# Performance work log

Measured on AMD Instinct MI355X. Metric: run time of the kernel, lower is better.

Reference implementation:

```python
import jax, jax.numpy as jnp
import numpy as np
from jax import lax

EPS = 2.220446049250313e-16  # np.finfo(float).eps, used in SparseDispatcher.combine
TOP_K = 2
LOSS_COEF = 1e-2


def _conv7(x, w, groups):
    # x: [B,C,H,W], w: [O, C//groups, 7, 7], 'same' padding
    return lax.conv_general_dilated(
        x, w, window_strides=(1, 1), padding=[(3, 3), (3, 3)],
        dimension_numbers=("NCHW", "OIHW", "NCHW"), feature_group_count=groups)


def setup_inputs() -> dict:
    key = jax.random.key(0)
    ks = jax.random.split(key, 8)
    B, C, H, E = 16, 64, 128, 8
    x = jax.random.normal(ks[0], (B, C, H, H), dtype=jnp.float32)
    # router: Conv2d(dim, 1, 7, padding=3)
    router_w = jax.random.normal(ks[1], (1, C, 7, 7), dtype=jnp.float32) * 0.05
    router_b = jnp.zeros((1,), dtype=jnp.float32)
    # gating weight: [weight_h*weight_h, num_experts] (small random so top-k is meaningful)
    w_gate = jax.random.normal(ks[2], (H * H, E), dtype=jnp.float32) * 0.01
    # experts: depthwise Conv2d(dim, dim, 7, groups=dim) per expert
    expert_w = jax.random.normal(ks[3], (E, C, 1, 7, 7), dtype=jnp.float32) * 0.05
    expert_b = jnp.zeros((E, C), dtype=jnp.float32)
    # shared expert: same depthwise conv
    shared_w = jax.random.normal(ks[4], (C, 1, 7, 7), dtype=jnp.float32) * 0.05
    shared_b = jnp.zeros((C,), dtype=jnp.float32)
    return dict(x=x, router_w=router_w, router_b=router_b, w_gate=w_gate,
                expert_w=expert_w, expert_b=expert_b,
                shared_w=shared_w, shared_b=shared_b)


def reference(x, router_w, router_b, w_gate, expert_w, expert_b, shared_w, shared_b):
    B, C, H, W = x.shape
    E = w_gate.shape[1]

    # ---- router + top-k gating (noisy_gating=False path) ----
    r = _conv7(x, router_w, groups=1) + router_b[None, :, None, None]   # [B,1,H,W]
    r_flat = r.reshape(B, H * W)                                        # [B,HW]
    logits = r_flat @ w_gate                                            # [B,E]
    top_logits, top_idx = lax.top_k(logits, min(TOP_K + 1, E))
    top_k_gates = jax.nn.softmax(top_logits[:, :TOP_K], axis=1)         # [B,k]
    gates = jnp.zeros((B, E), logits.dtype).at[
        jnp.arange(B)[:, None], top_idx[:, :TOP_K]].set(top_k_gates)     # [B,E]

    importance = gates.sum(0)
    load = (gates > 0).sum(0).astype(jnp.float32)

    def cv_sq(v):  # torch .var() is unbiased -> ddof=1
        return jnp.var(v, ddof=1) / (jnp.mean(v) ** 2 + 1e-10)

    loss = (cv_sq(importance) + cv_sq(load)) * LOSS_COEF

    # ---- experts: depthwise 7x7 conv per expert ----
    out = jax.vmap(lambda w, b: _conv7(x, w, C) + b[None, :, None, None])(
        expert_w, expert_b)                                             # [E,B,C,H,W]
    out = out.reshape(E, B, C, H * W).transpose(0, 1, 3, 2)             # [E,B,HW,C]

    # ---- SparseDispatcher.combine (multiply_by_gates=False): log-sum-exp over
    # selected experts only. Dense masked form == gather/scatter form exactly. ----
    mask = (gates > 0).T[:, :, None, None].astype(out.dtype)            # [E,B,1,1]
    combined = jnp.sum(jnp.exp(out) * mask, axis=0)                     # [B,HW,C]
    combined = jnp.where(combined == 0, EPS, combined)
    y = jnp.log(combined)

    # ---- shared expert ----
    shared = (_conv7(x, shared_w, C) + shared_b[None, :, None, None])
    shared = shared.reshape(B, C, H * W).transpose(0, 2, 1)             # [B,HW,C]

    return y + shared, loss
```

## Files before the change

### kernel.cpp

```cpp
#include <hip/hip_runtime.h>
#include <hip/hip_bf16.h>

#define B_  16
#define C_  64
#define H_  128
#define W_  128
#define HW_ (H_*W_)
#define E_  8

#define WS_LOGITS 0
#define WS_SEL    128
#define WS_PART   256

__global__ void k_sentinel(float* out, float v){
    if (blockIdx.x == 0 && threadIdx.x == 0) out[0] = v;
}

#define R_TH 16
#define R_TW 64
#define R_HH (R_TH+6)
#define R_HW (R_TW+6)
#define R_LS 76
#define R_HN (R_HH*R_HW)
#define RG_CH 8
#define RG_N  8

__device__ __forceinline__ void r_stage(const float* __restrict__ xc, float* dst,
                                        int row0, int col0, int tid){
    for (int i = tid; i < R_HN; i += 256){
        int hr = i / R_HW, hc = i - hr*R_HW;
        int gr = row0 + hr - 3, gc = col0 + hc - 3;
        float v = 0.f;
        if ((unsigned)gr < (unsigned)H_ && (unsigned)gc < (unsigned)W_)
            v = xc[gr*W_+gc];
        dst[hr*R_LS+hc] = v;
    }
}

__global__ __launch_bounds__(256) void k1p(const float* __restrict__ x,
                                           const float* __restrict__ rw,
                                           const float* __restrict__ rb,
                                           const float* __restrict__ wg,
                                           float* __restrict__ partial){
    __shared__ __align__(16) float tile[2][R_HH*R_LS];
    __shared__ float pred[4][E_];

    int id = blockIdx.x;
    int g   = id & 7; id >>= 3;
    int txt = id & 1; id >>= 1;
    int tyt = id & 7; id >>= 3;
    int b   = id;
    int row0 = tyt*R_TH, col0 = txt*R_TW;
    int tx = threadIdx.x & 15, ty = threadIdx.x >> 4;
    int row  = row0 + ty;
    int colb = col0 + 4*tx;

    const float* xg  = x  + ((size_t)(b*C_) + g*RG_CH)*HW_;
    const float* wgr = rw + g*RG_CH*49;

    float acc[4] = {0.f,0.f,0.f,0.f};

    r_stage(xg, tile[0], row0, col0, threadIdx.x);
    __syncthreads();

    for (int ch = 0; ch < RG_CH; ++ch){
        if (ch + 1 < RG_CH)
            r_stage(xg + (size_t)(ch+1)*HW_, tile[(ch+1)&1], row0, col0, threadIdx.x);

        const float* wr = wgr + ch*49;
        const float* tb = tile[ch&1];
        #pragma unroll
        for (int ky = 0; ky < 7; ++ky){
            const float* trp = &tb[(ty+ky)*R_LS + 4*tx];
            float4 va = *(const float4*)(trp);
            float4 vb = *(const float4*)(trp+4);
            float2 vc = *(const float2*)(trp+8);
            float win[10] = {va.x,va.y,va.z,va.w, vb.x,vb.y,vb.z,vb.w, vc.x,vc.y};
            #pragma unroll
            for (int kx = 0; kx < 7; ++kx){
                float w = wr[ky*7+kx];
                acc[0] += w*win[kx+0];
                acc[1] += w*win[kx+1];
                acc[2] += w*win[kx+2];
                acc[3] += w*win[kx+3];
            }
        }
        __syncthreads();
    }

    if (g == 0){
        float rbv = rb[0];
        acc[0]+=rbv; acc[1]+=rbv; acc[2]+=rbv; acc[3]+=rbv;
    }

    const float* wrow = wg + (size_t)(row*W_ + colb)*E_;
    float pl[E_];
    #pragma unroll
    for (int e = 0; e < E_; ++e) pl[e] = 0.f;
    #pragma unroll
    for (int p = 0; p < 4; ++p){
        float4 wa = *(const float4*)(wrow + p*E_);
        float4 wb = *(const float4*)(wrow + p*E_ + 4);
        float a = acc[p];
        pl[0] += a*wa.x; pl[1] += a*wa.y; pl[2] += a*wa.z; pl[3] += a*wa.w;
        pl[4] += a*wb.x; pl[5] += a*wb.y; pl[6] += a*wb.z; pl[7] += a*wb.w;
    }
    #pragma unroll
    for (int off = 32; off > 0; off >>= 1){
        #pragma unroll
        for (int e = 0; e < E_; ++e) pl[e] += __shfl_down(pl[e], off, 64);
    }
    int lane = threadIdx.x & 63, wv = threadIdx.x >> 6;
    if (lane == 0){
        #pragma unroll
        for (int e = 0; e < E_; ++e) pred[wv][e] = pl[e];
    }
    __syncthreads();
    if (threadIdx.x < E_){
        int e = threadIdx.x;
        float s = pred[0][e] + pred[1][e] + pred[2][e] + pred[3][e];
        partial[(size_t)blockIdx.x*E_ + e] = s;
    }
}

__global__ void k2_gating(const float* __restrict__ partial,
                          int* __restrict__ sel,
                          float* __restrict__ out){
    __shared__ float lg[B_*E_];
    __shared__ float g1s[B_], g2s[B_];
    __shared__ int   i1s[B_], i2s[B_];
    __shared__ float impS[E_], cntS[E_];
    int t = threadIdx.x;
    if (t < B_*E_){
        int b = t >> 3, e = t & 7;
        const float* pp = partial + ((size_t)b*128)*E_ + e;
        float s = 0.f;
        #pragma unroll 4
        for (int j = 0; j < 128; ++j) s += pp[(size_t)j*E_];
        lg[t] = s;
    }
    __syncthreads();
    if (t < B_){
        const float* l = lg + t*E_;
        int i1 = 0;
        #pragma unroll
        for (int e = 1; e < E_; ++e) if (l[e] > l[i1]) i1 = e;
        int i2 = (i1 == 0) ? 1 : 0;
        #pragma unroll
        for (int e = 0; e < E_; ++e) if (e != i1 && l[e] > l[i2]) i2 = e;
        float ex = expf(l[i2] - l[i1]);
        float g1 = 1.f/(1.f+ex), g2 = ex/(1.f+ex);
        sel[t] = i1; sel[B_ + t] = i2;
        g1s[t] = g1; g2s[t] = g2; i1s[t] = i1; i2s[t] = i2;
    }
    __syncthreads();
    if (t < E_){
        float im = 0.f, cn = 0.f;
        #pragma unroll
        for (int bb = 0; bb < B_; ++bb){
            im += (i1s[bb]==t ? g1s[bb] : 0.f) + (i2s[bb]==t ? g2s[bb] : 0.f);
            cn += (i1s[bb]==t ? 1.f : 0.f)     + (i2s[bb]==t ? 1.f : 0.f);
        }
        impS[t] = im; cntS[t] = cn;
    }
    __syncthreads();
    if (t == 0){
        float m1 = 0.f, m2 = 0.f;
        for (int e = 0; e < E_; ++e){ m1 += impS[e]; m2 += cntS[e]; }
        m1 *= (1.f/E_); m2 *= (1.f/E_);
        float v1 = 0.f, v2 = 0.f;
        for (int e = 0; e < E_; ++e){
            float d1 = impS[e] - m1; v1 += d1*d1;
            float d2 = cntS[e] - m2; v2 += d2*d2;
        }
        v1 *= (1.f/(E_-1)); v2 *= (1.f/(E_-1));
        float loss = (v1/(m1*m1 + 1e-10f) + v2/(m2*m2 + 1e-10f)) * 0.01f;
        out[(size_t)B_*HW_*C_] = loss;
    }
}

#define C3_NCH 8
#define C3_CS  28
#define C3_CHS 620
#define C3_WST 60
#define C3_TN  (C3_NCH*22*22)
#define C3_WN  (3*C3_NCH*C3_WST)

__global__ __launch_bounds__(256) void k3_tiled(const float* __restrict__ x,
                                                const float* __restrict__ ew,
                                                const float* __restrict__ eb,
                                                const float* __restrict__ sw,
                                                const float* __restrict__ sb,
                                                const int* __restrict__ sel,
                                                float* __restrict__ out){
    __shared__ __align__(16) float tile[C3_NCH*C3_CHS];
    __shared__ __align__(16) float wbuf[C3_WN];

    int id = blockIdx.x;
    int half = id & 1; id >>= 1;
    int cx = id & 7; id >>= 3;
    int cy = id & 7; id >>= 3;
    int b  = id;
    int r0 = cy*16, c0 = cx*16;

    int c8   = threadIdx.x & 7;
    int slot = threadIdx.x >> 3;
    int trow = slot >> 1;
    int colt = (slot & 1) * 8;

    int e1 = sel[b], e2 = sel[B_ + b];

    for (int kk = 0; kk < 4; ++kk){
        int cc0 = (half*4 + kk)*C3_NCH;
        __syncthreads();
        for (int i = threadIdx.x; i < C3_TN; i += 256){
            int ci = i / 484; int rem = i - ci*484;
            int hr = rem / 22, hc = rem - hr*22;
            int gr = r0 + hr - 3, gc = c0 + hc - 3;
            float v = 0.f;
            if ((unsigned)gr < (unsigned)H_ && (unsigned)gc < (unsigned)W_)
                v = x[((size_t)(b*C_ + cc0 + ci))*HW_ + gr*W_ + gc];
            tile[ci*C3_CHS + hr*C3_CS + hc] = v;
        }
        for (int i = threadIdx.x; i < C3_WN; i += 256){
            int which = i / (C3_NCH*C3_WST);
            int rem = i - which*(C3_NCH*C3_WST);
            int wc = rem / C3_WST;
            int tt = rem - wc*C3_WST;
            int ky = tt >> 3, kx = tt & 7;
            float v = 0.f;
            if (ky < 7 && kx < 7){
                int tap = ky*7 + kx;
                if (which == 0)      v = ew[((size_t)(e1*C_ + cc0 + wc))*49 + tap];
                else if (which == 1) v = ew[((size_t)(e2*C_ + cc0 + wc))*49 + tap];
                else                 v = sw[((size_t)(cc0 + wc))*49 + tap];
            }
            wbuf[i] = v;
        }
        __syncthreads();

        float a1[8], a2[8], a3[8];
        #pragma unroll
        for (int c = 0; c < 8; ++c){ a1[c]=0.f; a2[c]=0.f; a3[c]=0.f; }

        const float* tb = tile + c8*C3_CHS;
        #pragma unroll
        for (int ky = 0; ky < 7; ++ky){
            const float* trp = tb + (trow+ky)*C3_CS + colt;
            float win[16];
            #pragma unroll
            for (int q = 0; q < 4; ++q){
                float4 v4 = *(const float4*)(trp + 4*q);
                win[4*q+0]=v4.x; win[4*q+1]=v4.y; win[4*q+2]=v4.z; win[4*q+3]=v4.w;
            }
            float u1[7], u2[7], u3[7];
            { const float* wp = wbuf + (0*C3_NCH + c8)*C3_WST + ky*8;
              float4 a = *(const float4*)wp, c4 = *(const float4*)(wp+4);
              u1[0]=a.x;u1[1]=a.y;u1[2]=a.z;u1[3]=a.w;u1[4]=c4.x;u1[5]=c4.y;u1[6]=c4.z; }
            { const float* wp = wbuf + (1*C3_NCH + c8)*C3_WST + ky*8;
              float4 a = *(const float4*)wp, c4 = *(const float4*)(wp+4);
              u2[0]=a.x;u2[1]=a.y;u2[2]=a.z;u2[3]=a.w;u2[4]=c4.x;u2[5]=c4.y;u2[6]=c4.z; }
            { const float* wp = wbuf + (2*C3_NCH + c8)*C3_WST + ky*8;
              float4 a = *(const float4*)wp, c4 = *(const float4*)(wp+4);
              u3[0]=a.x;u3[1]=a.y;u3[2]=a.z;u3[3]=a.w;u3[4]=c4.x;u3[5]=c4.y;u3[6]=c4.z; }

            #pragma unroll
            for (int c = 0; c < 8; ++c){
                #pragma unroll
                for (int kx = 0; kx < 7; ++kx){
                    float xv = win[c+kx];
                    a1[c] += u1[kx]*xv;
                    a2[c] += u2[kx]*xv;
                    a3[c] += u3[kx]*xv;
                }
            }
        }

        float b1 = eb[e1*C_ + cc0 + c8];
        float b2 = eb[e2*C_ + cc0 + c8];
        float b3 = sb[cc0 + c8];
        size_t obase = ((size_t)b*HW_ + (size_t)(r0+trow)*W_ + (c0+colt))*C_ + cc0 + c8;
        #pragma unroll
        for (int c = 0; c < 8; ++c){
            float o1 = a1[c] + b1;
            float o2 = a2[c] + b2;
            float o3 = a3[c] + b3;
            float v = __expf(o1) + __expf(o2);
            if (v == 0.f) v = 2.220446049250313e-16f;
            out[obase + (size_t)c*C_] = __logf(v) + o3;
        }
    }
}

extern "C" void kernel_launch(void* const* d_in, const int* in_sizes, int n_in,
                              void* d_out, int out_size, void* d_ws, size_t ws_size,
                              hipStream_t stream) {
    float* out = (float*)d_out;

    static const int exp_sizes[8] = {16777216, 3136, 1, 131072, 25088, 512, 3136, 64};
    if (n_in != 8){ k_sentinel<<<1,64,0,stream>>>(out, 500.f); return; }
    for (int i = 0; i < 8; ++i){
        if (in_sizes[i] != exp_sizes[i]){
            k_sentinel<<<1,64,0,stream>>>(out, 600.f + 8.f*i); return;
        }
    }
    if (out_size != 16777217){ k_sentinel<<<1,64,0,stream>>>(out, 800.f); return; }
    if (ws_size < (size_t)(WS_PART + 2048*E_)*4){ k_sentinel<<<1,64,0,stream>>>(out, 900.f); return; }

    const float* x  = (const float*)d_in[0];
    const float* rw = (const float*)d_in[1];
    const float* rb = (const float*)d_in[2];
    const float* wg = (const float*)d_in[3];
    const float* ew = (const float*)d_in[4];
    const float* eb = (const float*)d_in[5];
    const float* sw = (const float*)d_in[6];
    const float* sb = (const float*)d_in[7];
    float* wsf = (float*)d_ws;

    k1p<<<2048, 256, 0, stream>>>(x, rw, rb, wg, wsf + WS_PART);
    k2_gating<<<1, 256, 0, stream>>>(wsf + WS_PART, (int*)(wsf + WS_SEL), out);
    k3_tiled<<<2048, 256, 0, stream>>>(x, ew, eb, sw, sb,
                                       (const int*)(wsf + WS_SEL), out);
}
```

Baseline: 311.6 us.

## Stage all router channels at once, precompute staging offsets, atomically reduce logits

The router kernel now loads all 8 channel planes into shared memory in one batched pass, using per-thread offsets computed once, and then runs the conv without per-channel barriers. The old double-buffered per-channel staging is removed. Partial logits are reduced with atomicAdd into a memset-zeroed buffer, so the gating kernel no longer sums 128 partials per logit. The expert kernel also precomputes its tile and weight gather offsets outside the channel loop. The cost is more shared memory and registers in the router kernel, an extra memset launch, and float atomics whose summation order is nondeterministic.

Result: slower. 325.1 us (+4.3%).

```diff
diff --git a/kernel.cpp b/kernel.cpp
--- a/kernel.cpp
+++ b/kernel.cpp
@@ -10,7 +10,6 @@
 
 #define WS_LOGITS 0
 #define WS_SEL    128
-#define WS_PART   256
 
 __global__ void k_sentinel(float* out, float v){
     if (blockIdx.x == 0 && threadIdx.x == 0) out[0] = v;
@@ -20,29 +19,18 @@
 #define R_TW 64
 #define R_HH (R_TH+6)
 #define R_HW (R_TW+6)
-#define R_LS 76
+#define R_LS 72
+#define R_PL (R_HH*R_LS)
 #define R_HN (R_HH*R_HW)
 #define RG_CH 8
-#define RG_N  8
-
-__device__ __forceinline__ void r_stage(const float* __restrict__ xc, float* dst,
-                                        int row0, int col0, int tid){
-    for (int i = tid; i < R_HN; i += 256){
-        int hr = i / R_HW, hc = i - hr*R_HW;
-        int gr = row0 + hr - 3, gc = col0 + hc - 3;
-        float v = 0.f;
-        if ((unsigned)gr < (unsigned)H_ && (unsigned)gc < (unsigned)W_)
-            v = xc[gr*W_+gc];
-        dst[hr*R_LS+hc] = v;
-    }
-}
+#define R_SL  7
 
 __global__ __launch_bounds__(256) void k1p(const float* __restrict__ x,
                                            const float* __restrict__ rw,
                                            const float* __restrict__ rb,
                                            const float* __restrict__ wg,
-                                           float* __restrict__ partial){
-    __shared__ __align__(16) float tile[2][R_HH*R_LS];
+                                           float* __restrict__ logits){
+    __shared__ __align__(16) float tile[RG_CH*R_PL];
     __shared__ float pred[4][E_];
 
     int id = blockIdx.x;
@@ -58,17 +46,40 @@
     const float* xg  = x  + ((size_t)(b*C_) + g*RG_CH)*HW_;
     const float* wgr = rw + g*RG_CH*49;
 
+    int goff[R_SL], loff[R_SL];
+    #pragma unroll
+    for (int q = 0; q < R_SL; ++q){
+        int i = (int)threadIdx.x + q*256;
+        goff[q] = -1; loff[q] = -1;
+        if (q < R_SL-1 || i < R_HN){
+            int hr = i / R_HW, hc = i - hr*R_HW;
+            loff[q] = hr*R_LS + hc;
+            int gr = row0 + hr - 3, gc = col0 + hc - 3;
+            if ((unsigned)gr < (unsigned)H_ && (unsigned)gc < (unsigned)W_)
+                goff[q] = gr*W_ + gc;
+        }
+    }
+
+    #pragma unroll
+    for (int ch = 0; ch < RG_CH; ++ch){
+        const float* xc = xg + (size_t)ch*HW_;
+        float v[R_SL];
+        #pragma unroll
+        for (int q = 0; q < R_SL; ++q){
+            v[q] = 0.f;
+            if (goff[q] >= 0) v[q] = xc[goff[q]];
+        }
+        #pragma unroll
+        for (int q = 0; q < R_SL; ++q)
+            if (loff[q] >= 0) tile[ch*R_PL + loff[q]] = v[q];
+    }
+    __syncthreads();
+
     float acc[4] = {0.f,0.f,0.f,0.f};
-
-    r_stage(xg, tile[0], row0, col0, threadIdx.x);
-    __syncthreads();
-
+    #pragma unroll
     for (int ch = 0; ch < RG_CH; ++ch){
-        if (ch + 1 < RG_CH)
-            r_stage(xg + (size_t)(ch+1)*HW_, tile[(ch+1)&1], row0, col0, threadIdx.x);
-
         const float* wr = wgr + ch*49;
-        const float* tb = tile[ch&1];
+        const float* tb = &tile[ch*R_PL];
         #pragma unroll
         for (int ky = 0; ky < 7; ++ky){
             const float* trp = &tb[(ty+ky)*R_LS + 4*tx];
@@ -85,7 +96,6 @@
                 acc[3] += w*win[kx+3];
             }
         }
-        __syncthreads();
     }
 
     if (g == 0){
@@ -119,29 +129,19 @@
     if (threadIdx.x < E_){
         int e = threadIdx.x;
         float s = pred[0][e] + pred[1][e] + pred[2][e] + pred[3][e];
-        partial[(size_t)blockIdx.x*E_ + e] = s;
-    }
-}
-
-__global__ void k2_gating(const float* __restrict__ partial,
+        atomicAdd(&logits[b*E_ + e], s);
+    }
+}
+
+__global__ void k2_gating(const float* __restrict__ logits,
                           int* __restrict__ sel,
                           float* __restrict__ out){
-    __shared__ float lg[B_*E_];
     __shared__ float g1s[B_], g2s[B_];
     __shared__ int   i1s[B_], i2s[B_];
     __shared__ float impS[E_], cntS[E_];
     int t = threadIdx.x;
-    if (t < B_*E_){
-        int b = t >> 3, e = t & 7;
-        const float* pp = partial + ((size_t)b*128)*E_ + e;
-        float s = 0.f;
-        #pragma unroll 4
-        for (int j = 0; j < 128; ++j) s += pp[(size_t)j*E_];
-        lg[t] = s;
-    }
-    __syncthreads();
     if (t < B_){
-        const float* l = lg + t*E_;
+        const float* l = logits + t*E_;
         int i1 = 0;
         #pragma unroll
         for (int e = 1; e < E_; ++e) if (l[e] > l[i1]) i1 = e;
@@ -185,6 +185,8 @@
 #define C3_WST 60
 #define C3_TN  (C3_NCH*22*22)
 #define C3_WN  (3*C3_NCH*C3_WST)
+#define C3_XS  16
+#define C3_WS  6
 
 __global__ __launch_bounds__(256) void k3_tiled(const float* __restrict__ x,
                                                 const float* __restrict__ ew,
@@ -210,32 +212,61 @@
 
     int e1 = sel[b], e2 = sel[B_ + b];
 
-    for (int kk = 0; kk < 4; ++kk){
-        int cc0 = (half*4 + kk)*C3_NCH;
-        __syncthreads();
-        for (int i = threadIdx.x; i < C3_TN; i += 256){
+    int xgo[C3_XS], xlo[C3_XS];
+    #pragma unroll
+    for (int q = 0; q < C3_XS; ++q){
+        int i = (int)threadIdx.x + q*256;
+        xgo[q] = -1; xlo[q] = -1;
+        if (q < C3_XS-1 || i < C3_TN){
             int ci = i / 484; int rem = i - ci*484;
             int hr = rem / 22, hc = rem - hr*22;
+            xlo[q] = ci*C3_CHS + hr*C3_CS + hc;
             int gr = r0 + hr - 3, gc = c0 + hc - 3;
-            float v = 0.f;
             if ((unsigned)gr < (unsigned)H_ && (unsigned)gc < (unsigned)W_)
-                v = x[((size_t)(b*C_ + cc0 + ci))*HW_ + gr*W_ + gc];
-            tile[ci*C3_CHS + hr*C3_CS + hc] = v;
-        }
-        for (int i = threadIdx.x; i < C3_WN; i += 256){
+                xgo[q] = ci*HW_ + gr*W_ + gc;
+        }
+    }
+    int wrel[C3_WS], wsel[C3_WS], wlo[C3_WS];
+    #pragma unroll
+    for (int q = 0; q < C3_WS; ++q){
+        int i = (int)threadIdx.x + q*256;
+        wrel[q] = -1; wsel[q] = 0; wlo[q] = -1;
+        if (q < C3_WS-1 || i < C3_WN){
             int which = i / (C3_NCH*C3_WST);
             int rem = i - which*(C3_NCH*C3_WST);
             int wc = rem / C3_WST;
             int tt = rem - wc*C3_WST;
             int ky = tt >> 3, kx = tt & 7;
-            float v = 0.f;
-            if (ky < 7 && kx < 7){
-                int tap = ky*7 + kx;
-                if (which == 0)      v = ew[((size_t)(e1*C_ + cc0 + wc))*49 + tap];
-                else if (which == 1) v = ew[((size_t)(e2*C_ + cc0 + wc))*49 + tap];
-                else                 v = sw[((size_t)(cc0 + wc))*49 + tap];
-            }
-            wbuf[i] = v;
+            wlo[q] = i; wsel[q] = which;
+            if (ky < 7 && kx < 7) wrel[q] = wc*49 + ky*7 + kx;
+        }
+    }
+
+    for (int kk = 0; kk < 4; ++kk){
+        int cc0 = (half*4 + kk)*C3_NCH;
+        __syncthreads();
+        const float* xb = x + (size_t)(b*C_ + cc0)*HW_;
+        #pragma unroll
+        for (int q = 0; q < C3_XS; ++q){
+            if (xlo[q] >= 0){
+                float v = 0.f;
+                if (xgo[q] >= 0) v = xb[xgo[q]];
+                tile[xlo[q]] = v;
+            }
+        }
+        const float* pe1 = ew + (size_t)(e1*C_ + cc0)*49;
+        const float* pe2 = ew + (size_t)(e2*C_ + cc0)*49;
+        const float* psw = sw + (size_t)cc0*49;
+        #pragma unroll
+        for (int q = 0; q < C3_WS; ++q){
+            if (wlo[q] >= 0){
+                float v = 0.f;
+                if (wrel[q] >= 0){
+                    const float* pw = (wsel[q]==0) ? pe1 : ((wsel[q]==1) ? pe2 : psw);
+                    v = pw[wrel[q]];
+                }
+                wbuf[wlo[q]] = v;
+            }
         }
         __syncthreads();
 
@@ -305,7 +336,7 @@
         }
     }
     if (out_size != 16777217){ k_sentinel<<<1,64,0,stream>>>(out, 800.f); return; }
-    if (ws_size < (size_t)(WS_PART + 2048*E_)*4){ k_sentinel<<<1,64,0,stream>>>(out, 900.f); return; }
+    if (ws_size < (size_t)(WS_SEL + 64)*4){ k_sentinel<<<1,64,0,stream>>>(out, 900.f); return; }
 
     const float* x  = (const float*)d_in[0];
     const float* rw = (const float*)d_in[1];
@@ -317,8 +348,9 @@
     const float* sb = (const float*)d_in[7];
     float* wsf = (float*)d_ws;
 
-    k1p<<<2048, 256, 0, stream>>>(x, rw, rb, wg, wsf + WS_PART);
-    k2_gating<<<1, 256, 0, stream>>>(wsf + WS_PART, (int*)(wsf + WS_SEL), out);
+    hipMemsetAsync(wsf + WS_LOGITS, 0, (B_*E_)*sizeof(float), stream);
+    k1p<<<2048, 256, 0, stream>>>(x, rw, rb, wg, wsf + WS_LOGITS);
+    k2_gating<<<1, 64, 0, stream>>>(wsf + WS_LOGITS, (int*)(wsf + WS_SEL), out);
     k3_tiled<<<2048, 256, 0, stream>>>(x, ew, eb, sw, sb,
                                        (const int*)(wsf + WS_SEL), out);
 }
```

## Fold router conv into gate weights and compute logits as a dot product

Applied to the files above, without the earlier changes.

Instead of running the 7x7 router convolution over x and then projecting onto w_gate, the router weights are first correlated with w_gate to form a per-channel, per-pixel, per-expert matrix G. The logits are then a plain dot product of x with G, and the bias term is handled separately through the column sums of w_gate. The aim is to replace the heavy per-batch convolution with a batch-independent precompute plus a streaming reduction over x. In exchange, G is written to and read back from the output buffer as scratch, which adds extra memory traffic. The reductions also rely on atomics, so summation order is no longer fixed.

Measured after the change: 772.3 us. 148% more time.

```diff
diff --git a/kernel.cpp b/kernel.cpp
--- a/kernel.cpp
+++ b/kernel.cpp
@@ -9,146 +9,155 @@
 #define E_  8
 
 #define WS_LOGITS 0
-#define WS_SEL    128
-#define WS_PART   256
+#define WS_S      128
+#define WS_SEL    160
 
 __global__ void k_sentinel(float* out, float v){
     if (blockIdx.x == 0 && threadIdx.x == 0) out[0] = v;
 }
 
-#define R_TH 16
-#define R_TW 64
-#define R_HH (R_TH+6)
-#define R_HW (R_TW+6)
-#define R_LS 76
-#define R_HN (R_HH*R_HW)
-#define RG_CH 8
-#define RG_N  8
-
-__device__ __forceinline__ void r_stage(const float* __restrict__ xc, float* dst,
-                                        int row0, int col0, int tid){
-    for (int i = tid; i < R_HN; i += 256){
-        int hr = i / R_HW, hc = i - hr*R_HW;
-        int gr = row0 + hr - 3, gc = col0 + hc - 3;
+#define GA_LS 24
+#define GA_PL (22*GA_LS)
+
+__global__ __launch_bounds__(256) void kA(const float* __restrict__ rw,
+                                          const float* __restrict__ wg,
+                                          float* __restrict__ g){
+    __shared__ float wgl[8*GA_PL];
+
+    int id = blockIdx.x;
+    int cg  = id & 7; id >>= 3;
+    int txT = id & 7; id >>= 3;
+    int tyT = id;
+    int qh0 = tyT*16, qw0 = txT*16;
+    int pxl = threadIdx.x & 15, py = threadIdx.x >> 4;
+
+    for (int i = threadIdx.x; i < 22*22*8; i += 256){
+        int pos = i >> 3, e = i & 7;
+        int hr = pos / 22, hc = pos - hr*22;
+        int r = qh0 - 3 + hr, c = qw0 - 3 + hc;
         float v = 0.f;
-        if ((unsigned)gr < (unsigned)H_ && (unsigned)gc < (unsigned)W_)
-            v = xc[gr*W_+gc];
-        dst[hr*R_LS+hc] = v;
-    }
-}
-
-__global__ __launch_bounds__(256) void k1p(const float* __restrict__ x,
-                                           const float* __restrict__ rw,
-                                           const float* __restrict__ rb,
-                                           const float* __restrict__ wg,
-                                           float* __restrict__ partial){
-    __shared__ __align__(16) float tile[2][R_HH*R_LS];
-    __shared__ float pred[4][E_];
-
-    int id = blockIdx.x;
-    int g   = id & 7; id >>= 3;
-    int txt = id & 1; id >>= 1;
-    int tyt = id & 7; id >>= 3;
-    int b   = id;
-    int row0 = tyt*R_TH, col0 = txt*R_TW;
-    int tx = threadIdx.x & 15, ty = threadIdx.x >> 4;
-    int row  = row0 + ty;
-    int colb = col0 + 4*tx;
-
-    const float* xg  = x  + ((size_t)(b*C_) + g*RG_CH)*HW_;
-    const float* wgr = rw + g*RG_CH*49;
-
-    float acc[4] = {0.f,0.f,0.f,0.f};
-
-    r_stage(xg, tile[0], row0, col0, threadIdx.x);
-    __syncthreads();
-
-    for (int ch = 0; ch < RG_CH; ++ch){
-        if (ch + 1 < RG_CH)
-            r_stage(xg + (size_t)(ch+1)*HW_, tile[(ch+1)&1], row0, col0, threadIdx.x);
-
-        const float* wr = wgr + ch*49;
-        const float* tb = tile[ch&1];
-        #pragma unroll
-        for (int ky = 0; ky < 7; ++ky){
-            const float* trp = &tb[(ty+ky)*R_LS + 4*tx];
-            float4 va = *(const float4*)(trp);
-            float4 vb = *(const float4*)(trp+4);
-            float2 vc = *(const float2*)(trp+8);
-            float win[10] = {va.x,va.y,va.z,va.w, vb.x,vb.y,vb.z,vb.w, vc.x,vc.y};
-            #pragma unroll
-            for (int kx = 0; kx < 7; ++kx){
-                float w = wr[ky*7+kx];
-                acc[0] += w*win[kx+0];
-                acc[1] += w*win[kx+1];
-                acc[2] += w*win[kx+2];
-                acc[3] += w*win[kx+3];
+        if ((unsigned)r < (unsigned)H_ && (unsigned)c < (unsigned)W_)
+            v = wg[(size_t)(r*W_ + c)*E_ + e];
+        wgl[e*GA_PL + hr*GA_LS + hc] = v;
+    }
+    __syncthreads();
+
+    float acc[8][8];
+    #pragma unroll
+    for (int ch = 0; ch < 8; ++ch)
+        #pragma unroll
+        for (int e = 0; e < 8; ++e) acc[ch][e] = 0.f;
+
+    const float* wr = rw + cg*8*49;
+    #pragma unroll
+    for (int ky = 0; ky < 7; ++ky){
+        #pragma unroll
+        for (int kx = 0; kx < 7; ++kx){
+            int base = (py + 6 - ky)*GA_LS + (pxl + 6 - kx);
+            float wgv[8];
+            #pragma unroll
+            for (int e = 0; e < 8; ++e) wgv[e] = wgl[e*GA_PL + base];
+            #pragma unroll
+            for (int ch = 0; ch < 8; ++ch){
+                float w = wr[ch*49 + ky*7 + kx];
+                #pragma unroll
+                for (int e = 0; e < 8; ++e) acc[ch][e] += w * wgv[e];
             }
         }
-        __syncthreads();
-    }
-
-    if (g == 0){
-        float rbv = rb[0];
-        acc[0]+=rbv; acc[1]+=rbv; acc[2]+=rbv; acc[3]+=rbv;
-    }
-
-    const float* wrow = wg + (size_t)(row*W_ + colb)*E_;
-    float pl[E_];
+    }
+
+    int q = (qh0 + py)*W_ + qw0 + pxl;
     #pragma unroll
-    for (int e = 0; e < E_; ++e) pl[e] = 0.f;
+    for (int ch = 0; ch < 8; ++ch){
+        size_t f = ((size_t)(cg*8 + ch)*HW_ + q)*E_;
+        *(float4*)(g + f)     = make_float4(acc[ch][0], acc[ch][1], acc[ch][2], acc[ch][3]);
+        *(float4*)(g + f + 4) = make_float4(acc[ch][4], acc[ch][5], acc[ch][6], acc[ch][7]);
+    }
+}
+
+__global__ __launch_bounds__(256) void kS(const float* __restrict__ wg,
+                                          float* __restrict__ S){
+    __shared__ float red[256];
+    int e = threadIdx.x & 7;
+    size_t base = (size_t)blockIdx.x*2048 + threadIdx.x;
+    float s = 0.f;
     #pragma unroll
-    for (int p = 0; p < 4; ++p){
-        float4 wa = *(const float4*)(wrow + p*E_);
-        float4 wb = *(const float4*)(wrow + p*E_ + 4);
-        float a = acc[p];
-        pl[0] += a*wa.x; pl[1] += a*wa.y; pl[2] += a*wa.z; pl[3] += a*wa.w;
-        pl[4] += a*wb.x; pl[5] += a*wb.y; pl[6] += a*wb.z; pl[7] += a*wb.w;
-    }
-    #pragma unroll
-    for (int off = 32; off > 0; off >>= 1){
-        #pragma unroll
-        for (int e = 0; e < E_; ++e) pl[e] += __shfl_down(pl[e], off, 64);
-    }
-    int lane = threadIdx.x & 63, wv = threadIdx.x >> 6;
-    if (lane == 0){
-        #pragma unroll
-        for (int e = 0; e < E_; ++e) pred[wv][e] = pl[e];
-    }
-    __syncthreads();
-    if (threadIdx.x < E_){
-        int e = threadIdx.x;
-        float s = pred[0][e] + pred[1][e] + pred[2][e] + pred[3][e];
-        partial[(size_t)blockIdx.x*E_ + e] = s;
-    }
-}
-
-__global__ void k2_gating(const float* __restrict__ partial,
+    for (int k = 0; k < 8; ++k) s += wg[base + k*256];
+    red[threadIdx.x] = s;
+    __syncthreads();
+    if (threadIdx.x < 8){
+        float t = 0.f;
+        #pragma unroll
+        for (int j = 0; j < 32; ++j) t += red[threadIdx.x + 8*j];
+        atomicAdd(&S[e], t);
+    }
+}
+
+#define KB_EP 1028
+
+__global__ __launch_bounds__(256) void kB(const float* __restrict__ x,
+                                          const float* __restrict__ g,
+                                          float* __restrict__ L){
+    __shared__ float gl[8*KB_EP];
+
+    size_t f0 = (size_t)blockIdx.x * 1024;
+    for (int i = threadIdx.x; i < 2048; i += 256){
+        float4 v = *(const float4*)(g + f0*E_ + (size_t)i*4);
+        int p = i >> 1, h = (i & 1)*4;
+        gl[(h+0)*KB_EP + p] = v.x;
+        gl[(h+1)*KB_EP + p] = v.y;
+        gl[(h+2)*KB_EP + p] = v.z;
+        gl[(h+3)*KB_EP + p] = v.w;
+    }
+    __syncthreads();
+
+    int w = threadIdx.x >> 6, l = threadIdx.x & 63;
+    for (int bb = 0; bb < 4; ++bb){
+        int b = bb*4 + w;
+        const float* xb = x + (size_t)b*(C_*HW_) + f0;
+        float acc[8];
+        #pragma unroll
+        for (int e = 0; e < 8; ++e) acc[e] = 0.f;
+        #pragma unroll
+        for (int k = 0; k < 16; ++k){
+            int pos = l + 64*k;
+            float xs = xb[pos];
+            #pragma unroll
+            for (int e = 0; e < 8; ++e) acc[e] += xs * gl[e*KB_EP + pos];
+        }
+        #pragma unroll
+        for (int off = 32; off > 0; off >>= 1){
+            #pragma unroll
+            for (int e = 0; e < 8; ++e) acc[e] += __shfl_down(acc[e], off, 64);
+        }
+        if (l == 0){
+            #pragma unroll
+            for (int e = 0; e < 8; ++e) atomicAdd(&L[b*E_ + e], acc[e]);
+        }
+    }
+}
+
+__global__ void k2_gating(const float* __restrict__ L,
+                          const float* __restrict__ S,
+                          const float* __restrict__ rb,
                           int* __restrict__ sel,
                           float* __restrict__ out){
-    __shared__ float lg[B_*E_];
     __shared__ float g1s[B_], g2s[B_];
     __shared__ int   i1s[B_], i2s[B_];
     __shared__ float impS[E_], cntS[E_];
     int t = threadIdx.x;
-    if (t < B_*E_){
-        int b = t >> 3, e = t & 7;
-        const float* pp = partial + ((size_t)b*128)*E_ + e;
-        float s = 0.f;
-        #pragma unroll 4
-        for (int j = 0; j < 128; ++j) s += pp[(size_t)j*E_];
-        lg[t] = s;
-    }
-    __syncthreads();
+    float rbv = rb[0];
     if (t < B_){
-        const float* l = lg + t*E_;
+        float le[E_];
+        #pragma unroll
+        for (int e = 0; e < E_; ++e) le[e] = L[t*E_ + e] + rbv*S[e];
         int i1 = 0;
         #pragma unroll
-        for (int e = 1; e < E_; ++e) if (l[e] > l[i1]) i1 = e;
+        for (int e = 1; e < E_; ++e) if (le[e] > le[i1]) i1 = e;
         int i2 = (i1 == 0) ? 1 : 0;
         #pragma unroll
-        for (int e = 0; e < E_; ++e) if (e != i1 && l[e] > l[i2]) i2 = e;
-        float ex = expf(l[i2] - l[i1]);
+        for (int e = 0; e < E_; ++e) if (e != i1 && le[e] > le[i2]) i2 = e;
+        float ex = expf(le[i2] - le[i1]);
         float g1 = 1.f/(1.f+ex), g2 = ex/(1.f+ex);
         sel[t] = i1; sel[B_ + t] = i2;
         g1s[t] = g1; g2s[t] = g2; i1s[t] = i1; i2s[t] = i2;
@@ -305,7 +314,7 @@
         }
     }
     if (out_size != 16777217){ k_sentinel<<<1,64,0,stream>>>(out, 800.f); return; }
-    if (ws_size < (size_t)(WS_PART + 2048*E_)*4){ k_sentinel<<<1,64,0,stream>>>(out, 900.f); return; }
+    if (ws_size < (size_t)(WS_SEL + 64)*4){ k_sentinel<<<1,64,0,stream>>>(out, 900.f); return; }
 
     const float* x  = (const float*)d_in[0];
     const float* rw = (const float*)d_in[1];
@@ -317,8 +326,12 @@
     const float* sb = (const float*)d_in[7];
     float* wsf = (float*)d_ws;
 
-    k1p<<<2048, 256, 0, stream>>>(x, rw, rb, wg, wsf + WS_PART);
-    k2_gating<<<1, 256, 0, stream>>>(wsf + WS_PART, (int*)(wsf + WS_SEL), out);
+    hipMemsetAsync(wsf, 0, (WS_S + E_)*sizeof(float), stream);
+    kA<<<512, 256, 0, stream>>>(rw, wg, out);
+    kS<<<64, 256, 0, stream>>>(wg, wsf + WS_S);
+    kB<<<1024, 256, 0, stream>>>(x, out, wsf + WS_LOGITS);
+    k2_gating<<<1, 64, 0, stream>>>(wsf + WS_LOGITS, wsf + WS_S, rb,
+                                    (int*)(wsf + WS_SEL), out);
     k3_tiled<<<2048, 256, 0, stream>>>(x, ew, eb, sw, sb,
                                        (const int*)(wsf + WS_SEL), out);
 }
```
